# Optimization experiments

Measured on AMD Instinct MI355X. Metric: run time of the kernel, lower is better.

Reference implementation:

```python
import jax, jax.numpy as jnp
import numpy as np


def _pair_table(L):
    # 0,0 0,1 ... upper-triangular (start,end) enumeration, P = L*(L+1)/2
    starts = np.concatenate([np.arange(i + 1) for i in range(L)])
    ends = np.concatenate([np.full(i + 1, i) for i in range(L)])
    return starts.astype(np.int32), ends.astype(np.int32)


def setup_inputs() -> dict:
    key = jax.random.key(0)
    ks = jax.random.split(key, 10)
    B, L, Q, H, T = 8, 384, 64, 256, 9
    p = lambda k, shape: jax.random.normal(k, shape, jnp.float32) * 0.02
    return dict(
        batch_hiddens=jax.random.normal(ks[0], (B, L, H), jnp.float32),
        batch_masks=jnp.ones((B, L), dtype=bool),
        queries=jax.random.normal(ks[1], (B, Q, H), jnp.float32),
        queries_locs=jax.random.uniform(ks[2], (B, Q, 2), jnp.float32) * L,
        queries_logits=jax.random.normal(ks[3], (B, Q, T + 1), jnp.float32),
        Wc=p(ks[4], (H, T + 1)), bc=jnp.zeros((T + 1,), jnp.float32),
        Wq=p(ks[5], (H, 2 * H)), bq=jnp.zeros((2 * H,), jnp.float32),
        Wv=p(ks[6], (H, 2 * H)), bv=jnp.zeros((2 * H,), jnp.float32),
        Wo=p(ks[7], (H, 2)), bo=jnp.zeros((2,), jnp.float32),
        Wf=p(ks[8], (H, 2)), bf=jnp.zeros((2,), jnp.float32),
    )


def reference(batch_hiddens, batch_masks, queries, queries_locs, queries_logits,
              Wc, bc, Wq, bq, Wv, bv, Wo, bo, Wf, bf):
    B, L, H = batch_hiddens.shape
    Q = queries.shape[1]
    starts, ends = _pair_table(L)  # static: L known at trace time

    # label probabilities: softmax(prior logits + classifier(queries))
    labels_pros = jax.nn.softmax(queries_logits + queries @ Wc + bc, axis=-1)

    # biaffine start/end channels
    qh = (queries @ Wq + bq).reshape(B, Q, 2, H)        # [B,Q,2,H]
    ch = (batch_hiddens @ Wv + bv).reshape(B, L, 2, H)  # [B,L,2,H]
    score = jnp.einsum('bqch,bvch->bcqv', qh, ch) / jnp.sqrt(jnp.float32(H))
    score = jnp.where(batch_masks[:, None, None, :], score, -1e8)

    # span score via start/end table gather: [B,Q,P]
    span = score[:, 0][:, :, starts] + score[:, 1][:, :, ends]
    mask_p = batch_masks[:, ends]  # [B,P] valid if end token valid

    # locator: gaussian distribution over spans centered at refined locations
    offset = queries @ Wo + bo                      # [B,Q,2]
    factors = jax.nn.softplus(queries @ Wf + bf)    # [B,Q,2] positive widths
    locs = queries_locs + offset                    # [B,Q,2]
    pairs_f = jnp.stack([jnp.asarray(starts), jnp.asarray(ends)], axis=-1).astype(jnp.float32)  # [P,2]
    d2 = (pairs_f[None, None] - locs[:, :, None]) ** 2          # [B,Q,P,2]
    weight = jnp.exp(-(d2 * factors[:, :, None]).sum(-1))       # [B,Q,P]
    weight = jnp.where(mask_p[:, None, :], weight, 0.0)

    # weighted softmax over spans
    m = jnp.max(span, axis=-1, keepdims=True)
    e = jnp.exp(span - m) * weight
    locs_pros = e / (jnp.sum(e, axis=-1, keepdims=True) + 1e-12)
    return labels_pros, locs_pros
```

## Files before the change

kernel.cpp:

```cpp
#include <hip/hip_runtime.h>
#include <math.h>

#define B_    8
#define L_    384
#define Q_    64
#define H_    256
#define R_    512
#define P_    73920
#define NF4   18480
#define QF4   4620

#define WS_WVT   0
#define WS_HIDT  131072
#define WS_QH    917504
#define WS_G     1179648
#define WS_LOCS  1441792
#define WS_FACT  1442816
#define WS_EXEY  1443840

__device__ __forceinline__ void tile_transpose(const float* __restrict__ in,
                                               float* __restrict__ outp,
                                               int M, int N, int mt, int nt,
                                               float* smem ) {
    float (*t)[65] = (float(*)[65])smem;
    int lane = threadIdx.x & 63, row4 = threadIdx.x >> 6;
    int m0 = mt * 64, n0 = nt * 64;
#pragma unroll
    for (int p = 0; p < 16; p++) {
        int m = m0 + p * 4 + row4;
        t[p * 4 + row4][lane] = in[m * N + n0 + lane];
    }
    __syncthreads();
#pragma unroll
    for (int p = 0; p < 16; p++) {
        int n = n0 + p * 4 + row4;
        outp[n * M + m0 + lane] = t[lane][p * 4 + row4];
    }
}

__global__ __launch_bounds__(256) void k_f1(const float* __restrict__ hid,
                                            const float* __restrict__ Wv,
                                            const float* __restrict__ queries,
                                            const float* __restrict__ Wq,
                                            const float* __restrict__ bq_p,
                                            const float* __restrict__ qlocs,
                                            const float* __restrict__ qlogits,
                                            const float* __restrict__ Wc,
                                            const float* __restrict__ bc,
                                            const float* __restrict__ Wo,
                                            const float* __restrict__ bo,
                                            const float* __restrict__ Wf,
                                            const float* __restrict__ bf,
                                            float* __restrict__ ws,
                                            float* __restrict__ out) {
    __shared__ float smem[64 * 65];
    int blk = blockIdx.x;
    int tid = threadIdx.x;

    if (blk < 192) {
        int b = blk / 24, t = blk % 24;
        int mt = t % 6, nt = t / 6;
        tile_transpose(hid + b * 98304, ws + WS_HIDT + b * 98304, 384, 256, mt, nt, smem);
        return;
    }
    if (blk < 224) {
        int t = blk - 192;
        int mt = t % 4, nt = t / 4;
        tile_transpose(Wv, ws + WS_WVT, 256, 512, mt, nt, smem);
        return;
    }
    if (blk < 352) {
        int row0 = (blk - 224) * 4;
        float (*q)[256] = (float(*)[256])smem;
        for (int i = tid; i < 1024; i += 256)
            q[i >> 8][i & 255] = queries[row0 * 256 + i];
        __syncthreads();
        float acc0[4] = {0, 0, 0, 0}, acc1[4] = {0, 0, 0, 0};
        int j0 = tid, j1 = tid + 256;
        for (int h = 0; h < 256; h += 2) {
            float wa0 = Wq[h * 512 + j0],       wa1 = Wq[h * 512 + j1];
            float wb0 = Wq[(h + 1) * 512 + j0], wb1 = Wq[(h + 1) * 512 + j1];
#pragma unroll
            for (int r = 0; r < 4; r++) {
                float qa = q[r][h], qb = q[r][h + 1];
                acc0[r] += qa * wa0 + qb * wb0;
                acc1[r] += qa * wa1 + qb * wb1;
            }
        }
        float b0 = bq_p[j0], b1 = bq_p[j1];
#pragma unroll
        for (int r = 0; r < 4; r++) {
            ws[WS_QH + (row0 + r) * 512 + j0] = acc0[r] + b0;
            ws[WS_QH + (row0 + r) * 512 + j1] = acc1[r] + b1;
        }
        return;
    }
    {
        int r = (blk - 352) * 4 + (tid >> 6);
        int lane = tid & 63;
        float q0 = queries[r * 256 + lane];
        float q1 = queries[r * 256 + lane + 64];
        float q2 = queries[r * 256 + lane + 128];
        float q3 = queries[r * 256 + lane + 192];

        float x[10];
#pragma unroll
        for (int t = 0; t < 10; t++) {
            float v = q0 * Wc[lane * 10 + t] + q1 * Wc[(lane + 64) * 10 + t]
                    + q2 * Wc[(lane + 128) * 10 + t] + q3 * Wc[(lane + 192) * 10 + t];
#pragma unroll
            for (int off = 32; off; off >>= 1) v += __shfl_xor(v, off);
            x[t] = qlogits[r * 10 + t] + bc[t] + v;
        }
        float m = -1e30f;
#pragma unroll
        for (int t = 0; t < 10; t++) m = fmaxf(m, x[t]);
        float s = 0.f;
#pragma unroll
        for (int t = 0; t < 10; t++) { x[t] = expf(x[t] - m); s += x[t]; }
        float inv = 1.0f / s;
        if (lane == 0) {
#pragma unroll
            for (int t = 0; t < 10; t++) out[r * 10 + t] = x[t] * inv;
        }

#pragma unroll
        for (int k = 0; k < 2; k++) {
            float vo = q0 * Wo[lane * 2 + k] + q1 * Wo[(lane + 64) * 2 + k]
                     + q2 * Wo[(lane + 128) * 2 + k] + q3 * Wo[(lane + 192) * 2 + k];
            float vf = q0 * Wf[lane * 2 + k] + q1 * Wf[(lane + 64) * 2 + k]
                     + q2 * Wf[(lane + 128) * 2 + k] + q3 * Wf[(lane + 192) * 2 + k];
#pragma unroll
            for (int off = 32; off; off >>= 1) { vo += __shfl_xor(vo, off); vf += __shfl_xor(vf, off); }
            if (lane == 0) {
                ws[WS_LOCS + r * 2 + k] = qlocs[r * 2 + k] + vo + bo[k];
                float xx = vf + bf[k];
                ws[WS_FACT + r * 2 + k] = (xx > 20.f) ? xx : log1pf(expf(xx));
            }
        }
    }
}

__global__ __launch_bounds__(512) void k_g(float* ws) {
    __shared__ float qh[8][512];
    int tid = threadIdx.x;
    int row0 = blockIdx.x * 8;
    for (int i = tid; i < 4096; i += 512)
        qh[i >> 9][i & 511] = ws[WS_QH + row0 * 512 + i];
    __syncthreads();
    int c = tid >> 8, h = tid & 255;
    const float* wvt = ws + WS_WVT + c * 65536 + h;
    float acc[8] = {0, 0, 0, 0, 0, 0, 0, 0};
    for (int hp = 0; hp < 256; hp += 4) {
        float w0 = wvt[(hp + 0) * 256];
        float w1 = wvt[(hp + 1) * 256];
        float w2 = wvt[(hp + 2) * 256];
        float w3 = wvt[(hp + 3) * 256];
#pragma unroll
        for (int r = 0; r < 8; r++) {
            float4 qv = *reinterpret_cast<const float4*>(&qh[r][c * 256 + hp]);
            acc[r] += qv.x * w0 + qv.y * w1 + qv.z * w2 + qv.w * w3;
        }
    }
#pragma unroll
    for (int r = 0; r < 8; r++)
        ws[WS_G + (row0 + r) * 512 + tid] = acc[r];
}

__device__ __forceinline__ float blockReduceMax(float v, float* red, int tid) {
    red[tid] = v; __syncthreads();
    for (int s = 128; s > 0; s >>= 1) {
        if (tid < s) red[tid] = fmaxf(red[tid], red[tid + s]);
        __syncthreads();
    }
    float r = red[0]; __syncthreads();
    return r;
}
__device__ __forceinline__ float blockReduceSum(float v, float* red, int tid) {
    red[tid] = v; __syncthreads();
    for (int s = 128; s > 0; s >>= 1) {
        if (tid < s) red[tid] += red[tid + s];
        __syncthreads();
    }
    float r = red[0]; __syncthreads();
    return r;
}

__global__ __launch_bounds__(256) void k_prep(const float* __restrict__ ws_c,
                                              float* __restrict__ ws,
                                              const int* __restrict__ mask,
                                              const float* __restrict__ bv) {
    __shared__ float g0[256], g1[256];
    __shared__ float s0[384], s1[384];
    __shared__ float Ex[384], Ey[384];
    __shared__ float ps[512];
    __shared__ float red[256];

    int tid = threadIdx.x;
    int r = blockIdx.x;
    int b = r >> 6;

    g0[tid] = ws_c[WS_G + r * 512 + tid];
    g1[tid] = ws_c[WS_G + r * 512 + 256 + tid];
    float lx = ws_c[WS_LOCS + r * 2 + 0], ly = ws_c[WS_LOCS + r * 2 + 1];
    float fx = ws_c[WS_FACT + r * 2 + 0], fy = ws_c[WS_FACT + r * 2 + 1];

    float p0v = ws_c[WS_QH + r * 512 + tid] * bv[tid];
    float p1v = ws_c[WS_QH + r * 512 + 256 + tid] * bv[256 + tid];
    float dotc0 = blockReduceSum(p0v, red, tid);
    float dotc1 = blockReduceSum(p1v, red, tid);
    __syncthreads();

    const float* hT = ws_c + WS_HIDT + b * 98304;
    {
        int v = tid;
        float a0 = 0.f, a1 = 0.f;
        const float* p = hT + v;
#pragma unroll 8
        for (int h = 0; h < 256; h++) {
            float x = p[h * 384];
            a0 += x * g0[h];
            a1 += x * g1[h];
        }
        bool mk = mask[b * 384 + v] != 0;
        s0[v] = mk ? (a0 + dotc0) * 0.0625f : -1e8f;
        s1[v] = mk ? (a1 + dotc1) * 0.0625f : -1e8f;
    }
    if (tid < 128) {
        int v = 256 + tid;
        float a0 = 0.f, a1 = 0.f;
        const float* p = hT + v;
#pragma unroll 8
        for (int h = 0; h < 256; h++) {
            float x = p[h * 384];
            a0 += x * g0[h];
            a1 += x * g1[h];
        }
        bool mk = mask[b * 384 + v] != 0;
        s0[v] = mk ? (a0 + dotc0) * 0.0625f : -1e8f;
        s1[v] = mk ? (a1 + dotc1) * 0.0625f : -1e8f;
    }
    __syncthreads();

    ps[tid] = s0[tid];
    ps[tid + 256] = (tid < 128) ? s0[tid + 256] : -1e30f;
    __syncthreads();
    for (int off = 1; off < 512; off <<= 1) {
        float a0 = (tid >= off) ? ps[tid - off] : -1e30f;
        float a1 = ps[tid + 256 - off];
        __syncthreads();
        ps[tid] = fmaxf(ps[tid], a0);
        ps[tid + 256] = fmaxf(ps[tid + 256], a1);
        __syncthreads();
    }
    float m0 = ps[383];
    float lm, lm1;
    { int e = tid; lm = s1[e] + ps[e]; lm1 = s1[e]; }
    if (tid < 128) { int e = tid + 256; lm = fmaxf(lm, s1[e] + ps[e]); lm1 = fmaxf(lm1, s1[e]); }
    float mM = blockReduceMax(lm, red, tid);
    float m1 = blockReduceMax(lm1, red, tid);

    {
        int i = tid;
        float ds = (float)i - lx;
        Ex[i] = expf(s0[i] - m0 - fx * ds * ds);
        float de = (float)i - ly;
        float mk = (mask[b * 384 + i] != 0) ? 1.f : 0.f;
        Ey[i] = mk * expf(s1[i] - m1 - fy * de * de);
    }
    if (tid < 128) {
        int i = tid + 256;
        float ds = (float)i - lx;
        Ex[i] = expf(s0[i] - m0 - fx * ds * ds);
        float de = (float)i - ly;
        float mk = (mask[b * 384 + i] != 0) ? 1.f : 0.f;
        Ey[i] = mk * expf(s1[i] - m1 - fy * de * de);
    }
    __syncthreads();

    ps[tid] = Ex[tid];
    ps[tid + 256] = (tid < 128) ? Ex[tid + 256] : 0.f;
    __syncthreads();
    for (int off = 1; off < 512; off <<= 1) {
        float a0 = (tid >= off) ? ps[tid - off] : 0.f;
        float a1 = ps[tid + 256 - off];
        __syncthreads();
        ps[tid] += a0;
        ps[tid + 256] += a1;
        __syncthreads();
    }
    float lsum = Ey[tid] * ps[tid];
    if (tid < 128) lsum += Ey[tid + 256] * ps[tid + 256];
    float S2 = blockReduceSum(lsum, red, tid);

    float C = expf(m0 + m1 - mM);
    float scale = C / (C * S2 + 1e-12f);

    float* exr = ws + WS_EXEY + r * 768;
    exr[tid]       = Ex[tid];
    exr[384 + tid] = Ey[tid] * scale;
    if (tid < 128) {
        exr[256 + tid] = Ex[256 + tid];
        exr[640 + tid] = Ey[256 + tid] * scale;
    }
}

__global__ __launch_bounds__(256) void k_write(const float* __restrict__ ws,
                                               float* __restrict__ out) {
    __shared__ float exey[768];
    int tid = threadIdx.x;
    int r = blockIdx.x >> 2, q = blockIdx.x & 3;
    const float* exr = ws + WS_EXEY + r * 768;
    for (int i = tid; i < 768; i += 256) exey[i] = exr[i];
    __syncthreads();
    const float* Ex = exey;
    const float* Ey = exey + 384;

    float* ob = out + 5120 + r * 73920;
    int base = q * QF4;
    int end = base + QF4;
    for (int idx = base + tid; idx < end; idx += 256) {
        int p0 = idx << 2;
        int e = (int)((sqrtf(8.f * (float)p0 + 1.f) - 1.f) * 0.5f);
        int tri = (e * (e + 1)) >> 1;
        while (tri > p0) { e--; tri -= (e + 1); }
        while (p0 - tri > e) { tri += (e + 1); e++; }
        int s = p0 - tri;
        float ey = Ey[e];
        float4 v;
        v.x = Ex[s] * ey; if (++s > e) { s = 0; ey = Ey[++e]; }
        v.y = Ex[s] * ey; if (++s > e) { s = 0; ey = Ey[++e]; }
        v.z = Ex[s] * ey; if (++s > e) { s = 0; ey = Ey[++e]; }
        v.w = Ex[s] * ey;
        reinterpret_cast<float4*>(ob)[idx] = v;
    }
}

extern "C" void kernel_launch(void* const* d_in, const int* in_sizes, int n_in,
                              void* d_out, int out_size, void* d_ws, size_t ws_size,
                              hipStream_t stream) {
    const float* hiddens = (const float*)d_in[0];
    const int* masks     = (const int*)d_in[1];
    const float* queries = (const float*)d_in[2];
    const float* qlocs   = (const float*)d_in[3];
    const float* qlogits = (const float*)d_in[4];
    const float* Wc = (const float*)d_in[5];
    const float* bc = (const float*)d_in[6];
    const float* Wq = (const float*)d_in[7];
    const float* bq = (const float*)d_in[8];
    const float* Wv = (const float*)d_in[9];
    const float* bv = (const float*)d_in[10];
    const float* Wo = (const float*)d_in[11];
    const float* bo = (const float*)d_in[12];
    const float* Wf = (const float*)d_in[13];
    const float* bf = (const float*)d_in[14];
    float* out = (float*)d_out;
    float* ws  = (float*)d_ws;

    hipLaunchKernelGGL(k_f1,    dim3(480),  dim3(256), 0, stream,
                       hiddens, Wv, queries, Wq, bq, qlocs, qlogits,
                       Wc, bc, Wo, bo, Wf, bf, ws, out);
    hipLaunchKernelGGL(k_g,     dim3(64),   dim3(512), 0, stream, ws);
    hipLaunchKernelGGL(k_prep,  dim3(512),  dim3(256), 0, stream, ws, ws, masks, bv);
    hipLaunchKernelGGL(k_write, dim3(2048), dim3(256), 0, stream, ws, out);
}
```

Baseline: 294.2 us.

## Fuse qh and G projections, use wavefront scans in prep kernel

Moves the queries@Wq projection, the qh·Wv^T product, the bias dot and the classifier/locator heads into one kernel (k_qhg). qh now stays in shared memory instead of going through global workspace, and k_front keeps only the transposes. k_prep now runs 384 threads, one per token. Its shared-memory Hillis-Steele scans and block reductions, each with many __syncthreads, are replaced by a single-wavefront scan using per-lane serial chunks and shuffles. The fused kernel launches only 128 blocks, so the front end has less parallelism, and the scans run on one wavefront while the other threads wait.

After: 242.1 us. 1.22x faster.

```diff
diff --git a/kernel.cpp b/kernel.cpp
--- a/kernel.cpp
+++ b/kernel.cpp
@@ -12,11 +12,11 @@
 
 #define WS_WVT   0
 #define WS_HIDT  131072
-#define WS_QH    917504
-#define WS_G     1179648
-#define WS_LOCS  1441792
-#define WS_FACT  1442816
-#define WS_EXEY  1443840
+#define WS_G     917504
+#define WS_DOTC  1179648
+#define WS_LOCS  1180672
+#define WS_FACT  1181696
+#define WS_EXEY  1182720
 
 __device__ __forceinline__ void tile_transpose(const float* __restrict__ in,
                                                float* __restrict__ outp,
@@ -38,180 +38,164 @@
     }
 }
 
-__global__ __launch_bounds__(256) void k_f1(const float* __restrict__ hid,
-                                            const float* __restrict__ Wv,
-                                            const float* __restrict__ queries,
-                                            const float* __restrict__ Wq,
-                                            const float* __restrict__ bq_p,
-                                            const float* __restrict__ qlocs,
-                                            const float* __restrict__ qlogits,
-                                            const float* __restrict__ Wc,
-                                            const float* __restrict__ bc,
-                                            const float* __restrict__ Wo,
-                                            const float* __restrict__ bo,
-                                            const float* __restrict__ Wf,
-                                            const float* __restrict__ bf,
-                                            float* __restrict__ ws,
-                                            float* __restrict__ out) {
+__global__ __launch_bounds__(256) void k_front(const float* __restrict__ hid,
+                                               const float* __restrict__ Wv,
+                                               float* __restrict__ ws) {
     __shared__ float smem[64 * 65];
     int blk = blockIdx.x;
-    int tid = threadIdx.x;
-
     if (blk < 192) {
         int b = blk / 24, t = blk % 24;
         int mt = t % 6, nt = t / 6;
         tile_transpose(hid + b * 98304, ws + WS_HIDT + b * 98304, 384, 256, mt, nt, smem);
-        return;
-    }
-    if (blk < 224) {
+    } else {
         int t = blk - 192;
         int mt = t % 4, nt = t / 4;
         tile_transpose(Wv, ws + WS_WVT, 256, 512, mt, nt, smem);
-        return;
-    }
-    if (blk < 352) {
-        int row0 = (blk - 224) * 4;
-        float (*q)[256] = (float(*)[256])smem;
-        for (int i = tid; i < 1024; i += 256)
-            q[i >> 8][i & 255] = queries[row0 * 256 + i];
-        __syncthreads();
-        float acc0[4] = {0, 0, 0, 0}, acc1[4] = {0, 0, 0, 0};
-        int j0 = tid, j1 = tid + 256;
+    }
+}
+
+__global__ __launch_bounds__(512) void k_qhg(const float* __restrict__ queries,
+                                             const float* __restrict__ Wq,
+                                             const float* __restrict__ bq_p,
+                                             const float* __restrict__ bv,
+                                             const float* __restrict__ qlocs,
+                                             const float* __restrict__ qlogits,
+                                             const float* __restrict__ Wc,
+                                             const float* __restrict__ bc,
+                                             const float* __restrict__ Wo,
+                                             const float* __restrict__ bo,
+                                             const float* __restrict__ Wf,
+                                             const float* __restrict__ bf,
+                                             float* __restrict__ ws,
+                                             float* __restrict__ out) {
+    __shared__ float q[4][256];
+    __shared__ float qh[4][512];
+    int tid = threadIdx.x;
+    int r0 = blockIdx.x * 4;
+
+    for (int i = tid; i < 1024; i += 512)
+        q[i >> 8][i & 255] = queries[r0 * 256 + i];
+    __syncthreads();
+
+    {
+        int j = tid;
+        float acc[4] = {0, 0, 0, 0};
         for (int h = 0; h < 256; h += 2) {
-            float wa0 = Wq[h * 512 + j0],       wa1 = Wq[h * 512 + j1];
-            float wb0 = Wq[(h + 1) * 512 + j0], wb1 = Wq[(h + 1) * 512 + j1];
-#pragma unroll
-            for (int r = 0; r < 4; r++) {
-                float qa = q[r][h], qb = q[r][h + 1];
-                acc0[r] += qa * wa0 + qb * wb0;
-                acc1[r] += qa * wa1 + qb * wb1;
+            float wa = Wq[h * 512 + j];
+            float wb = Wq[(h + 1) * 512 + j];
+#pragma unroll
+            for (int r = 0; r < 4; r++)
+                acc[r] += q[r][h] * wa + q[r][h + 1] * wb;
+        }
+        float bj = bq_p[j];
+#pragma unroll
+        for (int r = 0; r < 4; r++) qh[r][j] = acc[r] + bj;
+    }
+    __syncthreads();
+
+    {
+        int c = tid >> 8, h = tid & 255;
+        const float* wvt = ws + WS_WVT + c * 65536 + h;
+        float acc[4] = {0, 0, 0, 0};
+        for (int hp = 0; hp < 256; hp += 2) {
+            float w0 = wvt[hp * 256];
+            float w1 = wvt[(hp + 1) * 256];
+#pragma unroll
+            for (int r = 0; r < 4; r++)
+                acc[r] += qh[r][c * 256 + hp] * w0 + qh[r][c * 256 + hp + 1] * w1;
+        }
+#pragma unroll
+        for (int r = 0; r < 4; r++)
+            ws[WS_G + (r0 + r) * 512 + tid] = acc[r];
+    }
+
+    {
+        int w = tid >> 6, lane = tid & 63;
+        int r = w >> 1, c = w & 1;
+        float v = 0.f;
+#pragma unroll
+        for (int k = 0; k < 4; k++) {
+            int h = lane + 64 * k;
+            v += qh[r][c * 256 + h] * bv[c * 256 + h];
+        }
+#pragma unroll
+        for (int off = 32; off; off >>= 1) v += __shfl_xor(v, off);
+        if (lane == 0) ws[WS_DOTC + (r0 + r) * 2 + c] = v;
+    }
+
+    {
+        int w = tid >> 6, lane = tid & 63;
+        if (w < 4) {
+            int r = r0 + w;
+            float q0 = q[w][lane];
+            float q1 = q[w][lane + 64];
+            float q2 = q[w][lane + 128];
+            float q3 = q[w][lane + 192];
+
+            float x[10];
+#pragma unroll
+            for (int t = 0; t < 10; t++) {
+                float v = q0 * Wc[lane * 10 + t] + q1 * Wc[(lane + 64) * 10 + t]
+                        + q2 * Wc[(lane + 128) * 10 + t] + q3 * Wc[(lane + 192) * 10 + t];
+#pragma unroll
+                for (int off = 32; off; off >>= 1) v += __shfl_xor(v, off);
+                x[t] = qlogits[r * 10 + t] + bc[t] + v;
             }
-        }
-        float b0 = bq_p[j0], b1 = bq_p[j1];
-#pragma unroll
-        for (int r = 0; r < 4; r++) {
-            ws[WS_QH + (row0 + r) * 512 + j0] = acc0[r] + b0;
-            ws[WS_QH + (row0 + r) * 512 + j1] = acc1[r] + b1;
-        }
-        return;
-    }
-    {
-        int r = (blk - 352) * 4 + (tid >> 6);
-        int lane = tid & 63;
-        float q0 = queries[r * 256 + lane];
-        float q1 = queries[r * 256 + lane + 64];
-        float q2 = queries[r * 256 + lane + 128];
-        float q3 = queries[r * 256 + lane + 192];
-
-        float x[10];
-#pragma unroll
-        for (int t = 0; t < 10; t++) {
-            float v = q0 * Wc[lane * 10 + t] + q1 * Wc[(lane + 64) * 10 + t]
-                    + q2 * Wc[(lane + 128) * 10 + t] + q3 * Wc[(lane + 192) * 10 + t];
-#pragma unroll
-            for (int off = 32; off; off >>= 1) v += __shfl_xor(v, off);
-            x[t] = qlogits[r * 10 + t] + bc[t] + v;
-        }
-        float m = -1e30f;
-#pragma unroll
-        for (int t = 0; t < 10; t++) m = fmaxf(m, x[t]);
-        float s = 0.f;
-#pragma unroll
-        for (int t = 0; t < 10; t++) { x[t] = expf(x[t] - m); s += x[t]; }
-        float inv = 1.0f / s;
-        if (lane == 0) {
-#pragma unroll
-            for (int t = 0; t < 10; t++) out[r * 10 + t] = x[t] * inv;
-        }
-
-#pragma unroll
-        for (int k = 0; k < 2; k++) {
-            float vo = q0 * Wo[lane * 2 + k] + q1 * Wo[(lane + 64) * 2 + k]
-                     + q2 * Wo[(lane + 128) * 2 + k] + q3 * Wo[(lane + 192) * 2 + k];
-            float vf = q0 * Wf[lane * 2 + k] + q1 * Wf[(lane + 64) * 2 + k]
-                     + q2 * Wf[(lane + 128) * 2 + k] + q3 * Wf[(lane + 192) * 2 + k];
-#pragma unroll
-            for (int off = 32; off; off >>= 1) { vo += __shfl_xor(vo, off); vf += __shfl_xor(vf, off); }
+            float m = -1e30f;
+#pragma unroll
+            for (int t = 0; t < 10; t++) m = fmaxf(m, x[t]);
+            float s = 0.f;
+#pragma unroll
+            for (int t = 0; t < 10; t++) { x[t] = expf(x[t] - m); s += x[t]; }
+            float inv = 1.0f / s;
             if (lane == 0) {
-                ws[WS_LOCS + r * 2 + k] = qlocs[r * 2 + k] + vo + bo[k];
-                float xx = vf + bf[k];
-                ws[WS_FACT + r * 2 + k] = (xx > 20.f) ? xx : log1pf(expf(xx));
+#pragma unroll
+                for (int t = 0; t < 10; t++) out[r * 10 + t] = x[t] * inv;
             }
-        }
-    }
-}
-
-__global__ __launch_bounds__(512) void k_g(float* ws) {
-    __shared__ float qh[8][512];
-    int tid = threadIdx.x;
-    int row0 = blockIdx.x * 8;
-    for (int i = tid; i < 4096; i += 512)
-        qh[i >> 9][i & 511] = ws[WS_QH + row0 * 512 + i];
-    __syncthreads();
-    int c = tid >> 8, h = tid & 255;
-    const float* wvt = ws + WS_WVT + c * 65536 + h;
-    float acc[8] = {0, 0, 0, 0, 0, 0, 0, 0};
-    for (int hp = 0; hp < 256; hp += 4) {
-        float w0 = wvt[(hp + 0) * 256];
-        float w1 = wvt[(hp + 1) * 256];
-        float w2 = wvt[(hp + 2) * 256];
-        float w3 = wvt[(hp + 3) * 256];
-#pragma unroll
-        for (int r = 0; r < 8; r++) {
-            float4 qv = *reinterpret_cast<const float4*>(&qh[r][c * 256 + hp]);
-            acc[r] += qv.x * w0 + qv.y * w1 + qv.z * w2 + qv.w * w3;
-        }
-    }
-#pragma unroll
-    for (int r = 0; r < 8; r++)
-        ws[WS_G + (row0 + r) * 512 + tid] = acc[r];
-}
-
-__device__ __forceinline__ float blockReduceMax(float v, float* red, int tid) {
-    red[tid] = v; __syncthreads();
-    for (int s = 128; s > 0; s >>= 1) {
-        if (tid < s) red[tid] = fmaxf(red[tid], red[tid + s]);
-        __syncthreads();
-    }
-    float r = red[0]; __syncthreads();
-    return r;
-}
-__device__ __forceinline__ float blockReduceSum(float v, float* red, int tid) {
-    red[tid] = v; __syncthreads();
-    for (int s = 128; s > 0; s >>= 1) {
-        if (tid < s) red[tid] += red[tid + s];
-        __syncthreads();
-    }
-    float r = red[0]; __syncthreads();
-    return r;
-}
-
-__global__ __launch_bounds__(256) void k_prep(const float* __restrict__ ws_c,
+
+#pragma unroll
+            for (int k = 0; k < 2; k++) {
+                float vo = q0 * Wo[lane * 2 + k] + q1 * Wo[(lane + 64) * 2 + k]
+                         + q2 * Wo[(lane + 128) * 2 + k] + q3 * Wo[(lane + 192) * 2 + k];
+                float vf = q0 * Wf[lane * 2 + k] + q1 * Wf[(lane + 64) * 2 + k]
+                         + q2 * Wf[(lane + 128) * 2 + k] + q3 * Wf[(lane + 192) * 2 + k];
+#pragma unroll
+                for (int off = 32; off; off >>= 1) { vo += __shfl_xor(vo, off); vf += __shfl_xor(vf, off); }
+                if (lane == 0) {
+                    ws[WS_LOCS + r * 2 + k] = qlocs[r * 2 + k] + vo + bo[k];
+                    float xx = vf + bf[k];
+                    ws[WS_FACT + r * 2 + k] = (xx > 20.f) ? xx : log1pf(expf(xx));
+                }
+            }
+        }
+    }
+}
+
+__global__ __launch_bounds__(384) void k_prep(const float* __restrict__ ws_c,
                                               float* __restrict__ ws,
-                                              const int* __restrict__ mask,
-                                              const float* __restrict__ bv) {
+                                              const int* __restrict__ mask) {
     __shared__ float g0[256], g1[256];
     __shared__ float s0[384], s1[384];
     __shared__ float Ex[384], Ey[384];
-    __shared__ float ps[512];
-    __shared__ float red[256];
+    __shared__ float scal[4];
 
     int tid = threadIdx.x;
     int r = blockIdx.x;
     int b = r >> 6;
 
-    g0[tid] = ws_c[WS_G + r * 512 + tid];
-    g1[tid] = ws_c[WS_G + r * 512 + 256 + tid];
+    if (tid < 256) {
+        g0[tid] = ws_c[WS_G + r * 512 + tid];
+        g1[tid] = ws_c[WS_G + r * 512 + 256 + tid];
+    }
+    float dotc0 = ws_c[WS_DOTC + r * 2 + 0];
+    float dotc1 = ws_c[WS_DOTC + r * 2 + 1];
     float lx = ws_c[WS_LOCS + r * 2 + 0], ly = ws_c[WS_LOCS + r * 2 + 1];
     float fx = ws_c[WS_FACT + r * 2 + 0], fy = ws_c[WS_FACT + r * 2 + 1];
-
-    float p0v = ws_c[WS_QH + r * 512 + tid] * bv[tid];
-    float p1v = ws_c[WS_QH + r * 512 + 256 + tid] * bv[256 + tid];
-    float dotc0 = blockReduceSum(p0v, red, tid);
-    float dotc1 = blockReduceSum(p1v, red, tid);
     __syncthreads();
 
     const float* hT = ws_c + WS_HIDT + b * 98304;
+    float s0r, s1r;
+    bool mk;
     {
         int v = tid;
         float a0 = 0.f, a1 = 0.f;
@@ -222,87 +206,90 @@
             a0 += x * g0[h];
             a1 += x * g1[h];
         }
-        bool mk = mask[b * 384 + v] != 0;
-        s0[v] = mk ? (a0 + dotc0) * 0.0625f : -1e8f;
-        s1[v] = mk ? (a1 + dotc1) * 0.0625f : -1e8f;
-    }
-    if (tid < 128) {
-        int v = 256 + tid;
-        float a0 = 0.f, a1 = 0.f;
-        const float* p = hT + v;
-#pragma unroll 8
-        for (int h = 0; h < 256; h++) {
-            float x = p[h * 384];
-            a0 += x * g0[h];
-            a1 += x * g1[h];
-        }
-        bool mk = mask[b * 384 + v] != 0;
-        s0[v] = mk ? (a0 + dotc0) * 0.0625f : -1e8f;
-        s1[v] = mk ? (a1 + dotc1) * 0.0625f : -1e8f;
-    }
-    __syncthreads();
-
-    ps[tid] = s0[tid];
-    ps[tid + 256] = (tid < 128) ? s0[tid + 256] : -1e30f;
-    __syncthreads();
-    for (int off = 1; off < 512; off <<= 1) {
-        float a0 = (tid >= off) ? ps[tid - off] : -1e30f;
-        float a1 = ps[tid + 256 - off];
-        __syncthreads();
-        ps[tid] = fmaxf(ps[tid], a0);
-        ps[tid + 256] = fmaxf(ps[tid + 256], a1);
-        __syncthreads();
-    }
-    float m0 = ps[383];
-    float lm, lm1;
-    { int e = tid; lm = s1[e] + ps[e]; lm1 = s1[e]; }
-    if (tid < 128) { int e = tid + 256; lm = fmaxf(lm, s1[e] + ps[e]); lm1 = fmaxf(lm1, s1[e]); }
-    float mM = blockReduceMax(lm, red, tid);
-    float m1 = blockReduceMax(lm1, red, tid);
-
+        mk = mask[b * 384 + v] != 0;
+        s0r = mk ? (a0 + dotc0) * 0.0625f : -1e8f;
+        s1r = mk ? (a1 + dotc1) * 0.0625f : -1e8f;
+        s0[v] = s0r;
+        s1[v] = s1r;
+    }
+    __syncthreads();
+
+    if (tid < 64) {
+        int l = tid;
+        float p[6];
+        p[0] = s0[l * 6 + 0];
+#pragma unroll
+        for (int k = 1; k < 6; k++) p[k] = fmaxf(p[k - 1], s0[l * 6 + k]);
+        float run = p[5];
+#pragma unroll
+        for (int off = 1; off < 64; off <<= 1) {
+            float t = __shfl_up(run, off);
+            if (l >= off) run = fmaxf(run, t);
+        }
+        float excl = __shfl_up(run, 1);
+        if (l == 0) excl = -1e30f;
+        float m0 = __shfl(run, 63);
+        float lm = -1e30f, lm1 = -1e30f;
+#pragma unroll
+        for (int k = 0; k < 6; k++) {
+            float pm = fmaxf(excl, p[k]);
+            float sv = s1[l * 6 + k];
+            lm = fmaxf(lm, sv + pm);
+            lm1 = fmaxf(lm1, sv);
+        }
+#pragma unroll
+        for (int off = 1; off < 64; off <<= 1) {
+            lm  = fmaxf(lm,  __shfl_xor(lm,  off));
+            lm1 = fmaxf(lm1, __shfl_xor(lm1, off));
+        }
+        if (l == 0) { scal[0] = m0; scal[1] = lm1; scal[2] = lm; }
+    }
+    __syncthreads();
+
+    float m0 = scal[0], m1 = scal[1], mM = scal[2];
+    float exv, eyv;
     {
         int i = tid;
         float ds = (float)i - lx;
-        Ex[i] = expf(s0[i] - m0 - fx * ds * ds);
+        exv = expf(s0r - m0 - fx * ds * ds);
         float de = (float)i - ly;
-        float mk = (mask[b * 384 + i] != 0) ? 1.f : 0.f;
-        Ey[i] = mk * expf(s1[i] - m1 - fy * de * de);
-    }
-    if (tid < 128) {
-        int i = tid + 256;
-        float ds = (float)i - lx;
-        Ex[i] = expf(s0[i] - m0 - fx * ds * ds);
-        float de = (float)i - ly;
-        float mk = (mask[b * 384 + i] != 0) ? 1.f : 0.f;
-        Ey[i] = mk * expf(s1[i] - m1 - fy * de * de);
-    }
-    __syncthreads();
-
-    ps[tid] = Ex[tid];
-    ps[tid + 256] = (tid < 128) ? Ex[tid + 256] : 0.f;
-    __syncthreads();
-    for (int off = 1; off < 512; off <<= 1) {
-        float a0 = (tid >= off) ? ps[tid - off] : 0.f;
-        float a1 = ps[tid + 256 - off];
-        __syncthreads();
-        ps[tid] += a0;
-        ps[tid + 256] += a1;
-        __syncthreads();
-    }
-    float lsum = Ey[tid] * ps[tid];
-    if (tid < 128) lsum += Ey[tid + 256] * ps[tid + 256];
-    float S2 = blockReduceSum(lsum, red, tid);
-
-    float C = expf(m0 + m1 - mM);
-    float scale = C / (C * S2 + 1e-12f);
-
+        eyv = mk ? expf(s1r - m1 - fy * de * de) : 0.f;
+        Ex[i] = exv;
+        Ey[i] = eyv;
+    }
+    __syncthreads();
+
+    if (tid < 64) {
+        int l = tid;
+        float p[6];
+        p[0] = Ex[l * 6 + 0];
+#pragma unroll
+        for (int k = 1; k < 6; k++) p[k] = p[k - 1] + Ex[l * 6 + k];
+        float run = p[5];
+#pragma unroll
+        for (int off = 1; off < 64; off <<= 1) {
+            float t = __shfl_up(run, off);
+            if (l >= off) run += t;
+        }
+        float excl = __shfl_up(run, 1);
+        if (l == 0) excl = 0.f;
+        float s2l = 0.f;
+#pragma unroll
+        for (int k = 0; k < 6; k++)
+            s2l += Ey[l * 6 + k] * (excl + p[k]);
+#pragma unroll
+        for (int off = 1; off < 64; off <<= 1) s2l += __shfl_xor(s2l, off);
+        if (l == 0) {
+            float C = expf(m0 + m1 - mM);
+            scal[3] = C / (C * s2l + 1e-12f);
+        }
+    }
+    __syncthreads();
+
+    float scale = scal[3];
     float* exr = ws + WS_EXEY + r * 768;
-    exr[tid]       = Ex[tid];
-    exr[384 + tid] = Ey[tid] * scale;
-    if (tid < 128) {
-        exr[256 + tid] = Ex[256 + tid];
-        exr[640 + tid] = Ey[256 + tid] * scale;
-    }
+    exr[tid]       = exv;
+    exr[384 + tid] = eyv * scale;
 }
 
 __global__ __launch_bounds__(256) void k_write(const float* __restrict__ ws,
@@ -357,10 +344,9 @@
     float* out = (float*)d_out;
     float* ws  = (float*)d_ws;
 
-    hipLaunchKernelGGL(k_f1,    dim3(480),  dim3(256), 0, stream,
-                       hiddens, Wv, queries, Wq, bq, qlocs, qlogits,
-                       Wc, bc, Wo, bo, Wf, bf, ws, out);
-    hipLaunchKernelGGL(k_g,     dim3(64),   dim3(512), 0, stream, ws);
-    hipLaunchKernelGGL(k_prep,  dim3(512),  dim3(256), 0, stream, ws, ws, masks, bv);
+    hipLaunchKernelGGL(k_front, dim3(224),  dim3(256), 0, stream, hiddens, Wv, ws);
+    hipLaunchKernelGGL(k_qhg,   dim3(128),  dim3(512), 0, stream,
+                       queries, Wq, bq, bv, qlocs, qlogits, Wc, bc, Wo, bo, Wf, bf, ws, out);
+    hipLaunchKernelGGL(k_prep,  dim3(512),  dim3(384), 0, stream, ws, ws, masks);
     hipLaunchKernelGGL(k_write, dim3(2048), dim3(256), 0, stream, ws, out);
 }
```
